# Kernel tuning notes

Measured on AMD Instinct MI355X. Metric: run time of the kernel, lower is better.

## Reference

```python
import jax, jax.numpy as jnp
import numpy as np

B, IN_DIM, N_NODES, N_LEAVES, N_ACTIONS = 131072, 128, 511, 512, 16


def setup_inputs() -> dict:
    key = jax.random.key(0)
    k1, k2, k3, k4 = jax.random.split(key, 4)
    x = jax.random.normal(k1, (B, IN_DIM), dtype=jnp.float32)
    W1 = jax.random.normal(k2, (N_NODES, IN_DIM), dtype=jnp.float32) * 0.1
    b1 = jax.random.normal(k3, (N_NODES,), dtype=jnp.float32) * 0.1
    W2 = jax.random.normal(k4, (N_LEAVES, 2 * N_NODES), dtype=jnp.float32) * 0.05
    # leaf -> action assignment; arange % n_actions guarantees every group non-empty
    leaf_actions = (jnp.arange(N_LEAVES) % N_ACTIONS).astype(jnp.int32)
    return {"x": x, "W1": W1, "b1": b1, "W2": W2, "leaf_actions": leaf_actions}


def reference(x, W1, b1, W2, leaf_actions):
    # linear1
    h = x @ W1.T + b1                      # [B, N_NODES]
    # relu(h) || relu(-h)
    z = jnp.concatenate([jax.nn.relu(h), jax.nn.relu(-h)], axis=1)  # [B, 2*N_NODES]
    # linear2 (no bias)
    y = z @ W2.T                           # [B, N_LEAVES]
    # grouped segment-max over leaf columns, grouped by action id
    pooled = jax.ops.segment_max(y.T, leaf_actions, num_segments=N_ACTIONS).T  # [B, N_ACTIONS]
    return jax.nn.softmax(pooled, axis=-1)
```

## Files before the change

### kernel.cpp

```cpp
#include <hip/hip_runtime.h>
#include <hip/hip_bf16.h>

typedef unsigned short u16;
typedef unsigned int u32;
typedef __attribute__((ext_vector_type(8))) short bf16x8;
typedef __attribute__((ext_vector_type(4))) float f32x4;

#define NROWS   131072
#define KDIM    128
#define NNODES  511
#define NPAD    512
#define NACT    16

__device__ __forceinline__ u16 f2b(float v) {
  return __builtin_bit_cast(u16, __float2bfloat16(v));
}

union Frag {
  bf16x8 v;
  u16    u[8];
  int4   i;
  int    d[4];
};

__device__ __forceinline__ u32 encf(float f) {
  u32 b = __builtin_bit_cast(u32, f);
  return (b & 0x80000000u) ? ~b : (b | 0x80000000u);
}
__device__ __forceinline__ float decf(u32 u) {
  u32 b = (u & 0x80000000u) ? (u & 0x7FFFFFFFu) : ~u;
  return __builtin_bit_cast(float, b);
}

__global__ void prep_k(const float* __restrict__ W1, const float* __restrict__ W2,
                       const float* __restrict__ b1, u16* __restrict__ w1f,
                       u16* __restrict__ wdf, u16* __restrict__ wsf,
                       float* __restrict__ b1p, u32* __restrict__ outi) {
  int bid = blockIdx.x, t = threadIdx.x;
  if (bid < 256) {
    int o = bid * 256 + t;
    int j = o & 7, l = (o >> 3) & 63, kb = (o >> 9) & 3, nt = o >> 11;
    int row = nt * 16 + (l & 15);
    int col = kb * 32 + (l >> 4) * 8 + j;
    w1f[o] = f2b((row < NNODES) ? W1[row * KDIM + col] : 0.f);
  } else if (bid < 2304) {
    int isS = (bid >= 1280);
    int o = (bid - (isS ? 1280 : 256)) * 256 + t;
    int j = o & 7, l = (o >> 3) & 63, kb = (o >> 9) & 15, lt = o >> 13;
    int leaf = lt * 16 + (l & 15);
    int n = kb * 32 + (l >> 4) * 8 + j;
    float va = 0.f, vb = 0.f;
    if (n < NNODES) {
      va = W2[leaf * (2 * NNODES) + n];
      vb = W2[leaf * (2 * NNODES) + NNODES + n];
    }
    float v = isS ? 0.5f * (va + vb) : 0.5f * (va - vb);
    (isS ? wsf : wdf)[o] = f2b(v);
  } else if (bid < 2306) {
    int i = (bid - 2304) * 256 + t;
    if (i < NPAD) b1p[i] = (i < NNODES) ? b1[i] : 0.f;
  } else {
    int i = (bid - 2306) * 256 + t;
    ((uint4*)outi)[i] = make_uint4(0u, 0u, 0u, 0u);
  }
}

__global__ __launch_bounds__(256, 2) void gemm1_k(const float* __restrict__ x,
                                                  const u16* __restrict__ w1f,
                                                  const float* __restrict__ b1p,
                                                  u16* __restrict__ hb) {
  __shared__ u16 xs[4 * 4 * 64 * 8];
  __shared__ u16 hs[4 * 16 * 64 * 8];

  int t = threadIdx.x, wq = t >> 6, l = t & 63;
  int rg = blockIdx.x;
  int lm = l & 15, quad = l >> 4;

  {
    const float4* xg = (const float4*)(x + (size_t)rg * 64 * KDIM);
#pragma unroll
    for (int i = 0; i < 8; ++i) {
      int f = i * 256 + t;
      int row = f >> 5, col = (f & 31) * 4;
      float4 v = xg[f];
      ushort4 b;
      b.x = f2b(v.x); b.y = f2b(v.y); b.z = f2b(v.z); b.w = f2b(v.w);
      int rt = row >> 4, kb = col >> 5;
      int lane = (row & 15) + 16 * ((col >> 3) & 3);
      *(ushort4*)&xs[(((rt * 4 + kb) * 64 + lane) * 8) + (col & 7)] = b;
    }
  }
  __syncthreads();

  f32x4 zero4 = {0.f, 0.f, 0.f, 0.f};
  f32x4 acc[4][8];
#pragma unroll
  for (int rt = 0; rt < 4; ++rt)
#pragma unroll
    for (int ct = 0; ct < 8; ++ct) acc[rt][ct] = zero4;

#pragma unroll 1
  for (int kb = 0; kb < 4; ++kb) {
    Frag a[4];
#pragma unroll
    for (int rt = 0; rt < 4; ++rt)
      a[rt].i = *(const int4*)&xs[((rt * 4 + kb) * 64 + l) * 8];
#pragma unroll
    for (int ct = 0; ct < 8; ++ct) {
      Frag b;
      b.i = *(const int4*)(w1f + (((wq * 8 + ct) * 4 + kb) * 64 + l) * 8);
#pragma unroll
      for (int rt = 0; rt < 4; ++rt)
        acc[rt][ct] = __builtin_amdgcn_mfma_f32_16x16x32_bf16(a[rt].v, b.v, acc[rt][ct], 0, 0, 0);
    }
  }

#pragma unroll
  for (int ct = 0; ct < 8; ++ct) {
    int node = (wq * 8 + ct) * 16 + lm;
    float bias = b1p[node];
    int kb2 = node >> 5;
    int lsub = 16 * ((node >> 3) & 3);
    int j2 = node & 7;
#pragma unroll
    for (int rt = 0; rt < 4; ++rt)
#pragma unroll
      for (int r = 0; r < 4; ++r) {
        int rl = quad * 4 + r;
        hs[((rt * 16 + kb2) * 64 + (rl + lsub)) * 8 + j2] = f2b(acc[rt][ct][r] + bias);
      }
  }
  __syncthreads();

  {
    int4* dst = (int4*)(hb + (size_t)rg * 32768);
    const int4* src = (const int4*)hs;
#pragma unroll
    for (int i = 0; i < 16; ++i) dst[i * 256 + t] = src[i * 256 + t];
  }
}

__global__ __launch_bounds__(512, 2) void gemm2_k(const u16* __restrict__ hb,
                                                  const u16* __restrict__ wdf,
                                                  const u16* __restrict__ wsf,
                                                  u32* __restrict__ pooled) {
  int t = threadIdx.x, w = t >> 6, l = t & 63;
  int bid = blockIdx.x;
  int half = (bid >> 3) & 1;
  int rg2 = (bid & 7) | ((bid >> 4) << 3);
  int rh = w >> 1, wq = w & 1;
  int lm = l & 15, quad = l >> 4;

  const u16* hbase = hb  + ((size_t)(rg2 * 16 + rh * 4) * 16) * 512;
  const u16* dbase = wdf + ((size_t)(half * 16 + wq * 8) * 16) * 512;
  const u16* sbase = wsf + ((size_t)(half * 16 + wq * 8) * 16) * 512;

  f32x4 zero4 = {0.f, 0.f, 0.f, 0.f};
  f32x4 acc[4][8];
#pragma unroll
  for (int rt = 0; rt < 4; ++rt)
#pragma unroll
    for (int ct = 0; ct < 8; ++ct) acc[rt][ct] = zero4;

  Frag hA[4], hB[4], wA[8], wB[8];
#pragma unroll
  for (int rt = 0; rt < 4; ++rt)
    hA[rt].i = *(const int4*)(hbase + ((size_t)rt * 16 + 0) * 512 + l * 8);
#pragma unroll
  for (int ct = 0; ct < 8; ++ct)
    wA[ct].i = *(const int4*)(dbase + ((size_t)ct * 16 + 0) * 512 + l * 8);

#pragma unroll 1
  for (int kb = 0; kb < 16; kb += 2) {
#pragma unroll
    for (int ct = 0; ct < 8; ++ct)
      wB[ct].i = *(const int4*)(sbase + ((size_t)ct * 16 + kb) * 512 + l * 8);
#pragma unroll
    for (int rt = 0; rt < 4; ++rt)
      hB[rt].i = *(const int4*)(hbase + ((size_t)rt * 16 + kb + 1) * 512 + l * 8);
#pragma unroll
    for (int ct = 0; ct < 8; ++ct)
#pragma unroll
      for (int rt = 0; rt < 4; ++rt)
        acc[rt][ct] = __builtin_amdgcn_mfma_f32_16x16x32_bf16(hA[rt].v, wA[ct].v, acc[rt][ct], 0, 0, 0);
#pragma unroll
    for (int rt = 0; rt < 4; ++rt)
#pragma unroll
      for (int d = 0; d < 4; ++d) hA[rt].d[d] &= 0x7FFF7FFF;
#pragma unroll
    for (int ct = 0; ct < 8; ++ct)
      wA[ct].i = *(const int4*)(dbase + ((size_t)ct * 16 + kb + 1) * 512 + l * 8);
#pragma unroll
    for (int ct = 0; ct < 8; ++ct)
#pragma unroll
      for (int rt = 0; rt < 4; ++rt)
        acc[rt][ct] = __builtin_amdgcn_mfma_f32_16x16x32_bf16(hA[rt].v, wB[ct].v, acc[rt][ct], 0, 0, 0);

    int kn = (kb + 2) & 15;
#pragma unroll
    for (int ct = 0; ct < 8; ++ct)
      wB[ct].i = *(const int4*)(sbase + ((size_t)ct * 16 + kb + 1) * 512 + l * 8);
#pragma unroll
    for (int rt = 0; rt < 4; ++rt)
      hA[rt].i = *(const int4*)(hbase + ((size_t)rt * 16 + kn) * 512 + l * 8);
#pragma unroll
    for (int ct = 0; ct < 8; ++ct)
#pragma unroll
      for (int rt = 0; rt < 4; ++rt)
        acc[rt][ct] = __builtin_amdgcn_mfma_f32_16x16x32_bf16(hB[rt].v, wA[ct].v, acc[rt][ct], 0, 0, 0);
#pragma unroll
    for (int rt = 0; rt < 4; ++rt)
#pragma unroll
      for (int d = 0; d < 4; ++d) hB[rt].d[d] &= 0x7FFF7FFF;
#pragma unroll
    for (int ct = 0; ct < 8; ++ct)
      wA[ct].i = *(const int4*)(dbase + ((size_t)ct * 16 + kn) * 512 + l * 8);
#pragma unroll
    for (int ct = 0; ct < 8; ++ct)
#pragma unroll
      for (int rt = 0; rt < 4; ++rt)
        acc[rt][ct] = __builtin_amdgcn_mfma_f32_16x16x32_bf16(hB[rt].v, wB[ct].v, acc[rt][ct], 0, 0, 0);
  }

#pragma unroll
  for (int rt = 0; rt < 4; ++rt)
#pragma unroll
    for (int r = 0; r < 4; ++r) {
      float mx = acc[rt][0][r];
#pragma unroll
      for (int ct = 1; ct < 8; ++ct) mx = fmaxf(mx, acc[rt][ct][r]);
      int row = rg2 * 256 + rh * 64 + rt * 16 + quad * 4 + r;
      atomicMax(pooled + row * NACT + lm, encf(mx));
    }
}

__global__ void combine_k(u32* __restrict__ outi) {
  int row = blockIdx.x * 256 + threadIdx.x;
  uint4* p = (uint4*)(outi + (size_t)row * NACT);
  uint4 q[4];
#pragma unroll
  for (int i = 0; i < 4; ++i) q[i] = p[i];
  float v[NACT];
#pragma unroll
  for (int i = 0; i < 4; ++i) {
    v[i * 4 + 0] = decf(q[i].x); v[i * 4 + 1] = decf(q[i].y);
    v[i * 4 + 2] = decf(q[i].z); v[i * 4 + 3] = decf(q[i].w);
  }
  float m = v[0];
#pragma unroll
  for (int a = 1; a < NACT; ++a) m = fmaxf(m, v[a]);
  float s = 0.f;
#pragma unroll
  for (int a = 0; a < NACT; ++a) { float e = __expf(v[a] - m); v[a] = e; s += e; }
  float inv = 1.f / s;
  float4* pf = (float4*)(outi + (size_t)row * NACT);
#pragma unroll
  for (int i = 0; i < 4; ++i) {
    float4 o; o.x = v[i*4+0]*inv; o.y = v[i*4+1]*inv; o.z = v[i*4+2]*inv; o.w = v[i*4+3]*inv;
    pf[i] = o;
  }
}

extern "C" void kernel_launch(void* const* d_in, const int* in_sizes, int n_in,
                              void* d_out, int out_size, void* d_ws, size_t ws_size,
                              hipStream_t stream) {
  const float* x  = (const float*)d_in[0];
  const float* W1 = (const float*)d_in[1];
  const float* b1 = (const float*)d_in[2];
  const float* W2 = (const float*)d_in[3];

  char* ws = (char*)d_ws;
  u16*   hb  = (u16*)ws;
  u16*   w1f = (u16*)(ws + 134217728);
  u16*   wdf = (u16*)(ws + 134217728 + 131072);
  u16*   wsf = (u16*)(ws + 134217728 + 131072 + 524288);
  float* b1p = (float*)(ws + 134217728 + 131072 + 524288 + 524288);

  prep_k   <<<dim3(4354), dim3(256), 0, stream>>>(W1, W2, b1, w1f, wdf, wsf, b1p, (u32*)d_out);
  gemm1_k  <<<dim3(NROWS / 64), dim3(256), 0, stream>>>(x, w1f, b1p, hb);
  gemm2_k  <<<dim3(1024), dim3(512), 0, stream>>>(hb, wdf, wsf, (u32*)d_out);
  combine_k<<<dim3(NROWS / 256), dim3(256), 0, stream>>>((u32*)d_out);
}
```

Baseline: 278.5 us.

## Shrink gemm2 per-wave tile to 64x64 and double block count for occupancy

Each wave of gemm2 now computes a 4x4 block of 16x16 MFMA tiles instead of 4x8, and blocks cover 128 rows instead of 256, so the grid grows from 1024 to 2048 blocks. Launch bounds rise to 4 blocks per CU. The K loop is simplified to one k-block per iteration with single-buffered h fragments, where the old version alternated two buffers. The aim is to cut register pressure and raise occupancy so memory latency is hidden better. The cost is less operand reuse per wave (more global loads per MFMA), twice as many atomicMax calls per output, and less explicit prefetch overlap.

```diff
diff --git a/kernel.cpp b/kernel.cpp
--- a/kernel.cpp
+++ b/kernel.cpp
@@ -140,86 +140,65 @@
   }
 }
 
-__global__ __launch_bounds__(512, 2) void gemm2_k(const u16* __restrict__ hb,
+__global__ __launch_bounds__(512, 4) void gemm2_k(const u16* __restrict__ hb,
                                                   const u16* __restrict__ wdf,
                                                   const u16* __restrict__ wsf,
                                                   u32* __restrict__ pooled) {
   int t = threadIdx.x, w = t >> 6, l = t & 63;
   int bid = blockIdx.x;
   int half = (bid >> 3) & 1;
-  int rg2 = (bid & 7) | ((bid >> 4) << 3);
-  int rh = w >> 1, wq = w & 1;
+  int rg = (bid & 7) | ((bid >> 4) << 3);
+  int rh = w >> 2, wq = w & 3;
   int lm = l & 15, quad = l >> 4;
 
-  const u16* hbase = hb  + ((size_t)(rg2 * 16 + rh * 4) * 16) * 512;
-  const u16* dbase = wdf + ((size_t)(half * 16 + wq * 8) * 16) * 512;
-  const u16* sbase = wsf + ((size_t)(half * 16 + wq * 8) * 16) * 512;
+  const u16* hbase = hb  + ((size_t)(rg * 8 + rh * 4) * 16) * 512;
+  const u16* dbase = wdf + ((size_t)(half * 16 + wq * 4) * 16) * 512;
+  const u16* sbase = wsf + ((size_t)(half * 16 + wq * 4) * 16) * 512;
 
   f32x4 zero4 = {0.f, 0.f, 0.f, 0.f};
-  f32x4 acc[4][8];
-#pragma unroll
-  for (int rt = 0; rt < 4; ++rt)
-#pragma unroll
-    for (int ct = 0; ct < 8; ++ct) acc[rt][ct] = zero4;
-
-  Frag hA[4], hB[4], wA[8], wB[8];
-#pragma unroll
-  for (int rt = 0; rt < 4; ++rt)
-    hA[rt].i = *(const int4*)(hbase + ((size_t)rt * 16 + 0) * 512 + l * 8);
-#pragma unroll
-  for (int ct = 0; ct < 8; ++ct)
+  f32x4 acc[4][4];
+#pragma unroll
+  for (int rt = 0; rt < 4; ++rt)
+#pragma unroll
+    for (int ct = 0; ct < 4; ++ct) acc[rt][ct] = zero4;
+
+  Frag h4[4], wA[4], wB[4];
+#pragma unroll
+  for (int rt = 0; rt < 4; ++rt)
+    h4[rt].i = *(const int4*)(hbase + ((size_t)rt * 16 + 0) * 512 + l * 8);
+#pragma unroll
+  for (int ct = 0; ct < 4; ++ct)
     wA[ct].i = *(const int4*)(dbase + ((size_t)ct * 16 + 0) * 512 + l * 8);
+#pragma unroll
+  for (int ct = 0; ct < 4; ++ct)
+    wB[ct].i = *(const int4*)(sbase + ((size_t)ct * 16 + 0) * 512 + l * 8);
 
 #pragma unroll 1
-  for (int kb = 0; kb < 16; kb += 2) {
-#pragma unroll
-    for (int ct = 0; ct < 8; ++ct)
-      wB[ct].i = *(const int4*)(sbase + ((size_t)ct * 16 + kb) * 512 + l * 8);
-#pragma unroll
-    for (int rt = 0; rt < 4; ++rt)
-      hB[rt].i = *(const int4*)(hbase + ((size_t)rt * 16 + kb + 1) * 512 + l * 8);
-#pragma unroll
-    for (int ct = 0; ct < 8; ++ct)
+  for (int kb = 0; kb < 16; ++kb) {
+    int kn = (kb + 1) & 15;
+#pragma unroll
+    for (int ct = 0; ct < 4; ++ct)
 #pragma unroll
       for (int rt = 0; rt < 4; ++rt)
-        acc[rt][ct] = __builtin_amdgcn_mfma_f32_16x16x32_bf16(hA[rt].v, wA[ct].v, acc[rt][ct], 0, 0, 0);
-#pragma unroll
-    for (int rt = 0; rt < 4; ++rt)
-#pragma unroll
-      for (int d = 0; d < 4; ++d) hA[rt].d[d] &= 0x7FFF7FFF;
-#pragma unroll
-    for (int ct = 0; ct < 8; ++ct)
-      wA[ct].i = *(const int4*)(dbase + ((size_t)ct * 16 + kb + 1) * 512 + l * 8);
-#pragma unroll
-    for (int ct = 0; ct < 8; ++ct)
+        acc[rt][ct] = __builtin_amdgcn_mfma_f32_16x16x32_bf16(h4[rt].v, wA[ct].v, acc[rt][ct], 0, 0, 0);
+#pragma unroll
+    for (int rt = 0; rt < 4; ++rt)
+#pragma unroll
+      for (int d = 0; d < 4; ++d) h4[rt].d[d] &= 0x7FFF7FFF;
+#pragma unroll
+    for (int ct = 0; ct < 4; ++ct)
+      wA[ct].i = *(const int4*)(dbase + ((size_t)ct * 16 + kn) * 512 + l * 8);
+#pragma unroll
+    for (int ct = 0; ct < 4; ++ct)
 #pragma unroll
       for (int rt = 0; rt < 4; ++rt)
-        acc[rt][ct] = __builtin_amdgcn_mfma_f32_16x16x32_bf16(hA[rt].v, wB[ct].v, acc[rt][ct], 0, 0, 0);
-
-    int kn = (kb + 2) & 15;
-#pragma unroll
-    for (int ct = 0; ct < 8; ++ct)
-      wB[ct].i = *(const int4*)(sbase + ((size_t)ct * 16 + kb + 1) * 512 + l * 8);
-#pragma unroll
-    for (int rt = 0; rt < 4; ++rt)
-      hA[rt].i = *(const int4*)(hbase + ((size_t)rt * 16 + kn) * 512 + l * 8);
-#pragma unroll
-    for (int ct = 0; ct < 8; ++ct)
-#pragma unroll
-      for (int rt = 0; rt < 4; ++rt)
-        acc[rt][ct] = __builtin_amdgcn_mfma_f32_16x16x32_bf16(hB[rt].v, wA[ct].v, acc[rt][ct], 0, 0, 0);
-#pragma unroll
-    for (int rt = 0; rt < 4; ++rt)
-#pragma unroll
-      for (int d = 0; d < 4; ++d) hB[rt].d[d] &= 0x7FFF7FFF;
-#pragma unroll
-    for (int ct = 0; ct < 8; ++ct)
-      wA[ct].i = *(const int4*)(dbase + ((size_t)ct * 16 + kn) * 512 + l * 8);
-#pragma unroll
-    for (int ct = 0; ct < 8; ++ct)
-#pragma unroll
-      for (int rt = 0; rt < 4; ++rt)
-        acc[rt][ct] = __builtin_amdgcn_mfma_f32_16x16x32_bf16(hB[rt].v, wB[ct].v, acc[rt][ct], 0, 0, 0);
+        acc[rt][ct] = __builtin_amdgcn_mfma_f32_16x16x32_bf16(h4[rt].v, wB[ct].v, acc[rt][ct], 0, 0, 0);
+#pragma unroll
+    for (int ct = 0; ct < 4; ++ct)
+      wB[ct].i = *(const int4*)(sbase + ((size_t)ct * 16 + kn) * 512 + l * 8);
+#pragma unroll
+    for (int rt = 0; rt < 4; ++rt)
+      h4[rt].i = *(const int4*)(hbase + ((size_t)rt * 16 + kn) * 512 + l * 8);
   }
 
 #pragma unroll
@@ -228,8 +207,8 @@
     for (int r = 0; r < 4; ++r) {
       float mx = acc[rt][0][r];
 #pragma unroll
-      for (int ct = 1; ct < 8; ++ct) mx = fmaxf(mx, acc[rt][ct][r]);
-      int row = rg2 * 256 + rh * 64 + rt * 16 + quad * 4 + r;
+      for (int ct = 1; ct < 4; ++ct) mx = fmaxf(mx, acc[rt][ct][r]);
+      int row = rg * 128 + rh * 64 + rt * 16 + quad * 4 + r;
       atomicMax(pooled + row * NACT + lm, encf(mx));
     }
 }
@@ -278,6 +257,6 @@
 
   prep_k   <<<dim3(4354), dim3(256), 0, stream>>>(W1, W2, b1, w1f, wdf, wsf, b1p, (u32*)d_out);
   gemm1_k  <<<dim3(NROWS / 64), dim3(256), 0, stream>>>(x, w1f, b1p, hb);
-  gemm2_k  <<<dim3(1024), dim3(512), 0, stream>>>(hb, wdf, wsf, (u32*)d_out);
+  gemm2_k  <<<dim3(2048), dim3(512), 0, stream>>>(hb, wdf, wsf, (u32*)d_out);
   combine_k<<<dim3(NROWS / 256), dim3(256), 0, stream>>>((u32*)d_out);
 }
```

After: 277.0 us. About the same (-0.5%).
